# Performance work log

Hardware: AMD Instinct MI355X
Metric: run time of the kernel (lower is better)

Reference implementation:

```python
import jax, jax.numpy as jnp
import numpy as np

SCALE_BASE = 512.0
GAMMA = 0.96875

def xpos(x, downscale=False):
    # x: (B, L, d). XPOS = rotary embedding with exponential position-dependent scale.
    B, L, d = x.shape
    half = d // 2
    scale_vec = (jnp.arange(0, d, 2, dtype=jnp.float32) + 0.4 * d) / (1.4 * d)  # (half,)
    pos = jnp.arange(L, dtype=jnp.float32)
    scale = scale_vec[None, :] ** (pos[:, None] / SCALE_BASE)  # (L, half)
    if downscale:
        scale = 1.0 / scale
    inv_freq = 1.0 / (10000.0 ** (jnp.arange(half, dtype=jnp.float32) / half))
    sinusoid = pos[:, None] * inv_freq[None, :]  # (L, half)
    sin_s = jnp.repeat(jnp.sin(sinusoid) * scale, 2, axis=-1)  # duplicate_interleave -> (L, d)
    cos_s = jnp.repeat(jnp.cos(sinusoid) * scale, 2, axis=-1)
    x1, x2 = x[..., ::2], x[..., 1::2]
    rot = jnp.stack((-x2, x1), axis=-1).reshape(x.shape)  # rotate_every_two
    return x * cos_s + rot * sin_s

def decay_mask(L, gamma):
    n = jnp.arange(L)[:, None]
    m = jnp.arange(L)[None, :]
    diff = n - m
    expo = jnp.where(diff >= 0, diff, 0).astype(jnp.float32)
    return jnp.where(diff >= 0, gamma ** expo, 0.0)  # (L, L) causal decay

def setup_inputs() -> dict:
    key = jax.random.key(0)
    kx, kq, kk, kv = jax.random.split(key, 4)
    B, L, H = 4, 2048, 1024
    hs = 1024  # head_size == v_dim
    X = jax.random.normal(kx, (B, L, H), dtype=jnp.float32)
    W_Q = jax.random.normal(kq, (H, hs), dtype=jnp.float32) / H
    W_K = jax.random.normal(kk, (H, hs), dtype=jnp.float32) / H
    W_V = jax.random.normal(kv, (H, hs), dtype=jnp.float32) / H
    return {"X": X, "W_Q": W_Q, "W_K": W_K, "W_V": W_V}

def reference(X, W_Q, W_K, W_V):
    L = X.shape[1]
    Q = xpos(X @ W_Q)
    K = xpos(X @ W_K, downscale=True)
    V = X @ W_V
    D = decay_mask(L, GAMMA)
    ret = jnp.einsum('bnd,bmd->bnm', Q, K) * D[None]  # (B, L, L)
    return ret @ V
```

## Files before the change

### kernel.cpp

```cpp
#include <hip/hip_runtime.h>
#include <cmath>

typedef __attribute__((ext_vector_type(8))) short short8;
typedef __attribute__((ext_vector_type(4))) short short4v;
typedef __attribute__((ext_vector_type(4))) float float4v;
typedef unsigned short ushort_t;

#define LSEQ   2048
#define DMODEL 1024
#define BM 128
#define BN 128
#define BK 64
#define TPAD 136

#define L2GAMMA (-0.045803595f)
#define L2E4_512 (0.0259525632f)

__device__ __forceinline__ ushort_t f2b(float x) {
    union { float f; unsigned u; } v; v.f = x;
    unsigned r = v.u + 0x7fffu + ((v.u >> 16) & 1u);
    return (ushort_t)(r >> 16);
}

#define GLOAD_LDS16(gptr, lptr)                                                     \
    __builtin_amdgcn_global_load_lds(                                               \
        (const __attribute__((address_space(1))) unsigned int*)(gptr),              \
        (__attribute__((address_space(3))) unsigned int*)(lptr), 16, 0, 0)

#define MFMA16 __builtin_amdgcn_mfma_f32_16x16x32_bf16

__device__ __forceinline__ void gemm16_core(
    const ushort_t* __restrict__ Ag, int lda, int aRow0,
    const ushort_t* __restrict__ Bg, int ldb, int bRow0,
    int kDepth, ushort_t* As, ushort_t* Bs, float4v acc[4][4])
{
    const int tid  = threadIdx.x;
    const int wave = tid >> 6, lane = tid & 63;
    const int wm = wave >> 1, wn = wave & 1;
    const int l15 = lane & 15, l4g = lane >> 4, l7 = lane & 7;
    const int srow = lane >> 3;
    const int scol = ((lane & 7) ^ srow) * 8;

    const ushort_t* ap[4];
    const ushort_t* bp[4];
    #pragma unroll
    for (int L = 0; L < 4; ++L) {
        int r = (wave * 4 + L) * 8 + srow;
        ap[L] = Ag + (size_t)(aRow0 + r) * lda + scol;
        bp[L] = Bg + (size_t)(bRow0 + r) * ldb + scol;
    }
    const int ldst = srow * BK + (lane & 7) * 8;

    int aBase[2], bBase[2];
    #pragma unroll
    for (int h = 0; h < 2; ++h) {
        const int ch = ((h * 4 + l4g) ^ l7) * 8;
        aBase[h] = (wm * 64 + l15) * BK + ch;
        bBase[h] = (wn * 64 + l15) * BK + ch;
    }

    const int nt = kDepth / BK;
    #pragma unroll
    for (int L = 0; L < 4; ++L) {
        GLOAD_LDS16(ap[L], As + (wave * 4 + L) * (8 * BK) + ldst);
        GLOAD_LDS16(bp[L], Bs + (wave * 4 + L) * (8 * BK) + ldst);
        ap[L] += BK; bp[L] += BK;
    }

    for (int j = 0; j < nt; ++j) {
        const int cur = (j & 1) * (BM * BK);
        const int nxt = ((j + 1) & 1) * (BM * BK);
        if (j + 1 < nt) {
            #pragma unroll
            for (int L = 0; L < 4; ++L) {
                GLOAD_LDS16(ap[L], As + nxt + (wave * 4 + L) * (8 * BK) + ldst);
                GLOAD_LDS16(bp[L], Bs + nxt + (wave * 4 + L) * (8 * BK) + ldst);
                ap[L] += BK; bp[L] += BK;
            }
            asm volatile("s_waitcnt vmcnt(8)" ::: "memory");
        } else {
            asm volatile("s_waitcnt vmcnt(0)" ::: "memory");
        }
        __builtin_amdgcn_s_barrier();
        asm volatile("" ::: "memory");

        #pragma unroll
        for (int h = 0; h < 2; ++h) {
            short8 a[4], b[4];
            #pragma unroll
            for (int f = 0; f < 4; ++f) {
                a[f] = *(const short8*)(As + cur + aBase[h] + f * (16 * BK));
                b[f] = *(const short8*)(Bs + cur + bBase[h] + f * (16 * BK));
            }
            #pragma unroll
            for (int fr = 0; fr < 4; ++fr)
                #pragma unroll
                for (int fc = 0; fc < 4; ++fc)
                    acc[fr][fc] = MFMA16(a[fr], b[fc], acc[fr][fc], 0, 0, 0);
        }
        asm volatile("" ::: "memory");
        __builtin_amdgcn_s_barrier();
    }
}

__global__ __launch_bounds__(256) void prep_kernel(
    float2* __restrict__ T,
    const float* __restrict__ Wq, const float* __restrict__ Wk,
    const float* __restrict__ Wv, ushort_t* __restrict__ Wt,
    const float4* __restrict__ X, short4v* __restrict__ Xb, int n4)
{
    __shared__ float t[32][33];
    const int bid = blockIdx.x;
    if (bid < 8192) {
        int idx = bid * 256 + threadIdx.x;
        int l = idx & 2047;
        int p = (idx >> 11) & 511;
        int mode = idx >> 20;
        float sv = (2.0f * (float)p + 409.6f) * (1.0f / 1433.6f);
        float coeff = log2f(sv) * (1.0f / 512.0f) + L2GAMMA;
        float invf = exp2f(-(float)p * L2E4_512);
        float lf = (float)l;
        float s, c;
        sincosf(lf * invf, &s, &c);
        float g = exp2f((mode == 0 ? lf : -lf) * coeff);
        T[idx] = make_float2(c * g, s * g);
    } else if (bid < 11264) {
        const int wb = bid - 8192;
        const int bz = wb >> 10;
        const int rem = wb & 1023;
        const int by = rem >> 5, bx = rem & 31;
        const float* W = bz == 0 ? Wq : bz == 1 ? Wk : Wv;
        ushort_t* O = Wt + (size_t)bz * (DMODEL * DMODEL);
        const int x = threadIdx.x & 31, y = (threadIdx.x >> 5) * 4;
        const int k0 = by * 32, n0 = bx * 32;
        #pragma unroll
        for (int j = 0; j < 4; ++j)
            t[y + j][x] = W[(size_t)(k0 + y + j) * DMODEL + n0 + x];
        __syncthreads();
        #pragma unroll
        for (int j = 0; j < 4; ++j)
            O[(size_t)(n0 + y + j) * DMODEL + k0 + x] = f2b(t[x][y + j]);
    } else {
        int i = (bid - 11264) * 256 + threadIdx.x;
        if (i < n4) {
            float4 v = X[i];
            short4v o;
            o.x = (short)f2b(v.x); o.y = (short)f2b(v.y);
            o.z = (short)f2b(v.z); o.w = (short)f2b(v.w);
            Xb[i] = o;
        }
    }
}

__global__ __launch_bounds__(256) void qkv16_kernel(
    const ushort_t* __restrict__ Xb, const ushort_t* __restrict__ Wt,
    const float2* __restrict__ Tab,
    ushort_t* __restrict__ Q, ushort_t* __restrict__ Ko, ushort_t* __restrict__ Vt)
{
    __shared__ ushort_t smem[32768];
    ushort_t* As = smem;
    ushort_t* Bs = smem + 16384;

    const int nwg = gridDim.x;
    const int orig = blockIdx.x;
    const int lin = (orig & 7) * (nwg >> 3) + (orig >> 3);
    const int inner = lin & 63;
    const int sup = lin >> 6;
    const int c = (sup % 3) * 8 + (inner & 7);
    const int r = (sup / 3) * 8 + (inner >> 3);
    const int mode = c >> 3;
    const int c0 = (c & 7) * BN;
    const int row0 = r * BM;

    const int tid = threadIdx.x;
    const int wave = tid >> 6, lane = tid & 63;
    const int wm = wave >> 1, wn = wave & 1;
    const int l15 = lane & 15, l4g = lane >> 4, l7 = lane & 7;

    const int srow = lane >> 3;
    const int scol = ((lane & 7) ^ srow) * 8;
    const char* gA = (const char*)Xb;
    const char* gB = (const char*)(Wt + (size_t)mode * (DMODEL * DMODEL));
    unsigned aoff[4], boff[4];
    #pragma unroll
    for (int L = 0; L < 4; ++L) {
        const int rr = (wave * 4 + L) * 8 + srow;
        aoff[L] = (unsigned)(((row0 + rr) * DMODEL + scol) * 2);
        boff[L] = (unsigned)(((c0 + rr) * DMODEL + scol) * 2);
    }
    const int ldst = srow * BK + (lane & 7) * 8;

    int aBase[2], bBase[2];
    #pragma unroll
    for (int h = 0; h < 2; ++h) {
        const int ch = ((h * 4 + l4g) ^ l7) * 8;
        aBase[h] = (wm * 64 + l15) * BK + ch;
        bBase[h] = (wn * 64 + l15) * BK + ch;
    }

    float4v acc[4][4] = {};

    #pragma unroll
    for (int L = 0; L < 4; ++L) {
        GLOAD_LDS16(gA + aoff[L], As + (wave * 4 + L) * (8 * BK) + ldst);
        GLOAD_LDS16(gB + boff[L], Bs + (wave * 4 + L) * (8 * BK) + ldst);
        aoff[L] += 2 * BK; boff[L] += 2 * BK;
    }

    #pragma unroll 2
    for (int k = 0; k < 16; ++k) {
        const int cur = (k & 1) * (BM * BK);
        const int nxt = ((k + 1) & 1) * (BM * BK);
        if (k < 15) {
            #pragma unroll
            for (int L = 0; L < 4; ++L) {
                GLOAD_LDS16(gA + aoff[L], As + nxt + (wave * 4 + L) * (8 * BK) + ldst);
                GLOAD_LDS16(gB + boff[L], Bs + nxt + (wave * 4 + L) * (8 * BK) + ldst);
                aoff[L] += 2 * BK; boff[L] += 2 * BK;
            }
            asm volatile("s_waitcnt vmcnt(8)" ::: "memory");
        } else {
            asm volatile("s_waitcnt vmcnt(0)" ::: "memory");
        }
        __builtin_amdgcn_s_barrier();
        asm volatile("" ::: "memory");

        #pragma unroll
        for (int h = 0; h < 2; ++h) {
            short8 a[4], b[4];
            #pragma unroll
            for (int f = 0; f < 4; ++f) {
                a[f] = *(const short8*)(As + cur + aBase[h] + f * (16 * BK));
                b[f] = *(const short8*)(Bs + cur + bBase[h] + f * (16 * BK));
            }
            #pragma unroll
            for (int fr = 0; fr < 4; ++fr)
                #pragma unroll
                for (int fc = 0; fc < 4; ++fc)
                    acc[fr][fc] = MFMA16(a[fr], b[fc], acc[fr][fc], 0, 0, 0);
        }
        asm volatile("" ::: "memory");
        __builtin_amdgcn_s_barrier();
    }

    const int rB = row0 + wm * 64 + l4g * 4;
    const int cB = c0 + wn * 64 + l15;

    if (mode < 2) {
        ushort_t* O = (mode == 0) ? Q : Ko;
        const float2* Tm = Tab + (size_t)mode * (512 * 2048);
        #pragma unroll
        for (int fc = 0; fc < 4; ++fc) {
            const int col = cB + fc * 16;
            const float2* tp = Tm + ((size_t)(col >> 1) << 11);
            #pragma unroll
            for (int fr = 0; fr < 4; ++fr) {
                const int row = rB + fr * 16;
                const int l0 = row & 2047;
                float4 t01 = *(const float4*)(tp + l0);
                float4 t23 = *(const float4*)(tp + l0 + 2);
                float cs[8] = {t01.x, t01.y, t01.z, t01.w,
                               t23.x, t23.y, t23.z, t23.w};
                #pragma unroll
                for (int q = 0; q < 4; ++q) {
                    float v  = acc[fc][0][0];
                    v = acc[fr][fc][q];
                    float pv = __shfl_xor(v, 1);
                    float cc = cs[2 * q], ss = cs[2 * q + 1];
                    float res = (lane & 1) ? fmaf(v, cc, pv * ss)
                                           : fmaf(v, cc, -pv * ss);
                    O[(size_t)(row + q) * DMODEL + col] = f2b(res);
                }
            }
        }
    } else {
        __syncthreads();
        #pragma unroll
        for (int fc = 0; fc < 4; ++fc)
            #pragma unroll
            for (int fr = 0; fr < 4; ++fr) {
                short4v pk;
                pk.x = (short)f2b(acc[fr][fc][0]);
                pk.y = (short)f2b(acc[fr][fc][1]);
                pk.z = (short)f2b(acc[fr][fc][2]);
                pk.w = (short)f2b(acc[fr][fc][3]);
                *(short4v*)(smem + (wn * 64 + fc * 16 + l15) * TPAD
                                 + wm * 64 + fr * 16 + l4g * 4) = pk;
            }
        __syncthreads();
        const int t = threadIdx.x;
        const int colV = c0 + (t >> 1);
        const int lhalf = (t & 1) * 64;
        const int b = row0 >> 11, lpos0 = (row0 & 2047) + lhalf;
        #pragma unroll
        for (int i = 0; i < 8; ++i) {
            short8 vv = *(const short8*)(smem + (t >> 1) * TPAD + lhalf + i * 8);
            *(short8*)(Vt + (size_t)b * (LSEQ * DMODEL)
                          + (size_t)colV * LSEQ + lpos0 + i * 8) = vv;
        }
    }
}

__global__ __launch_bounds__(256) void score_kernel(
    const ushort_t* __restrict__ Q, const ushort_t* __restrict__ Kc,
    ushort_t* __restrict__ S)
{
    const int t = blockIdx.x, z = blockIdx.z;
    int bi, bj;
    if (t < 3) { bi = (t > 0); bj = t - (t > 0); }
    else { int u = t - 3; bi = 2 + u / 3; bj = bi - 2 + u % 3; }

    __shared__ ushort_t As[2 * BM * BK], Bs[2 * BN * BK];
    float4v acc[4][4] = {};
    const size_t zoff = (size_t)z * (LSEQ * DMODEL);
    gemm16_core(Q + zoff, DMODEL, bi * BM, Kc + zoff, DMODEL, bj * BN,
                DMODEL, As, Bs, acc);

    const int wave = threadIdx.x >> 6, lane = threadIdx.x & 63;
    const int wm = wave >> 1, wn = wave & 1;
    const int l15 = lane & 15, l4g = lane >> 4;
    const int nB = bi * BM + wm * 64 + l4g * 4;
    const int mB = bj * BN + wn * 64 + l15;
    ushort_t* Sz = S + (size_t)z * LSEQ * LSEQ;
    #pragma unroll
    for (int fr = 0; fr < 4; ++fr)
        #pragma unroll
        for (int fc = 0; fc < 4; ++fc) {
            const int m = mB + fc * 16;
            #pragma unroll
            for (int q = 0; q < 4; ++q) {
                const int n = nB + fr * 16 + q;
                Sz[(size_t)n * LSEQ + m] =
                    (m <= n) ? f2b(acc[fr][fc][q]) : (ushort_t)0;
            }
        }
}

__global__ __launch_bounds__(256) void av_kernel(
    const ushort_t* __restrict__ S, const ushort_t* __restrict__ Vt,
    float* __restrict__ Out)
{
    const int bx = blockIdx.x, bi = blockIdx.y, z = blockIdx.z;
    const int kLo = (bi >= 2) ? (bi - 2) * BM : 0;
    const int kW  = (bi + 1) * BM - kLo;
    __shared__ ushort_t As[2 * BM * BK], Bs[2 * BN * BK];
    float4v acc[4][4] = {};
    gemm16_core(S + (size_t)z * LSEQ * LSEQ + kLo, LSEQ, bi * BM,
                Vt + (size_t)z * (LSEQ * DMODEL) + kLo, LSEQ, bx * BN,
                kW, As, Bs, acc);

    const int wave = threadIdx.x >> 6, lane = threadIdx.x & 63;
    const int wm = wave >> 1, wn = wave & 1;
    const int l15 = lane & 15, l4g = lane >> 4;
    const int rB = bi * BM + wm * 64 + l4g * 4;
    const int cB = bx * BN + wn * 64 + l15;
    float* Oz = Out + (size_t)z * (LSEQ * DMODEL);
    #pragma unroll
    for (int fr = 0; fr < 4; ++fr)
        #pragma unroll
        for (int fc = 0; fc < 4; ++fc)
            #pragma unroll
            for (int q = 0; q < 4; ++q)
                Oz[(size_t)(rB + fr * 16 + q) * DMODEL + cB + fc * 16] =
                    acc[fr][fc][q];
}

extern "C" void kernel_launch(void* const* d_in, const int* in_sizes, int n_in,
                              void* d_out, int out_size, void* d_ws, size_t ws_size,
                              hipStream_t stream)
{
    const float* X  = (const float*)d_in[0];
    const float* Wq = (const float*)d_in[1];
    const float* Wk = (const float*)d_in[2];
    const float* Wv = (const float*)d_in[3];
    float* out = (float*)d_out;

    const size_t LH  = (size_t)LSEQ * DMODEL;
    const size_t WSZ = (size_t)DMODEL * DMODEL;
    const size_t SSZ = (size_t)LSEQ * LSEQ;
    const size_t TABN = (size_t)2 * 512 * 2048;

    size_t need4 = TABN * 8 + 2 * (3 * WSZ + 4 * (4 * LH + SSZ));
    const int bs = (ws_size >= need4) ? 4 : 1;

    float2* Tab = (float2*)d_ws;
    ushort_t* ws16 = (ushort_t*)(Tab + TABN);
    ushort_t* Wt = ws16;
    ushort_t* Xb = Wt + 3 * WSZ;
    ushort_t* Q  = Xb + (size_t)bs * LH;
    ushort_t* Kb = Q  + (size_t)bs * LH;
    ushort_t* Vt = Kb + (size_t)bs * LH;
    ushort_t* S  = Vt + (size_t)bs * LH;

    if (bs == 4) {
        prep_kernel<<<dim3(19456), 256, 0, stream>>>(
            Tab, Wq, Wk, Wv, Wt, (const float4*)X, (short4v*)Xb,
            (int)(4 * LH / 4));
        qkv16_kernel<<<dim3(24 * 4 * 16), 256, 0, stream>>>(
            Xb, Wt, Tab, Q, Kb, Vt);
        score_kernel<<<dim3(45, 1, 4), 256, 0, stream>>>(Q, Kb, S);
        av_kernel<<<dim3(8, 16, 4), 256, 0, stream>>>(S, Vt, out);
    } else {
        prep_kernel<<<dim3(11264), 256, 0, stream>>>(
            Tab, Wq, Wk, Wv, Wt, (const float4*)X, (short4v*)Xb, 0);
        for (int p = 0; p < 4; ++p) {
            const float* Xp = X + (size_t)p * LH;
            prep_kernel<<<dim3(2048), 256, 0, stream>>>(
                Tab, Wq, Wk, Wv, Wt,
                (const float4*)Xp, (short4v*)Xb, (int)(LH / 4));
            qkv16_kernel<<<dim3(24 * 16), 256, 0, stream>>>(
                Xb, Wt, Tab, Q, Kb, Vt);
            score_kernel<<<dim3(45, 1, 1), 256, 0, stream>>>(Q, Kb, S);
            av_kernel<<<dim3(8, 16, 1), 256, 0, stream>>>(S, Vt,
                out + (size_t)p * LH);
        }
    }
}
```

Baseline: 196.5 us.

## Split score tiles into 64-row blocks and stage AV output through LDS

```diff
diff --git a/kernel.cpp b/kernel.cpp
--- a/kernel.cpp
+++ b/kernel.cpp
@@ -263,8 +263,7 @@
                                t23.x, t23.y, t23.z, t23.w};
                 #pragma unroll
                 for (int q = 0; q < 4; ++q) {
-                    float v  = acc[fc][0][0];
-                    v = acc[fr][fc][q];
+                    float v  = acc[fr][fc][q];
                     float pv = __shfl_xor(v, 1);
                     float cc = cs[2 * q], ss = cs[2 * q + 1];
                     float res = (lane & 1) ? fmaf(v, cc, pv * ss)
@@ -306,24 +305,96 @@
     ushort_t* __restrict__ S)
 {
     const int t = blockIdx.x, z = blockIdx.z;
-    int bi, bj;
-    if (t < 3) { bi = (t > 0); bj = t - (t > 0); }
-    else { int u = t - 3; bi = 2 + u / 3; bj = bi - 2 + u % 3; }
-
-    __shared__ ushort_t As[2 * BM * BK], Bs[2 * BN * BK];
-    float4v acc[4][4] = {};
-    const size_t zoff = (size_t)z * (LSEQ * DMODEL);
-    gemm16_core(Q + zoff, DMODEL, bi * BM, Kc + zoff, DMODEL, bj * BN,
-                DMODEL, As, Bs, acc);
-
-    const int wave = threadIdx.x >> 6, lane = threadIdx.x & 63;
+    int ri, tj;
+    if (t < 2)      { ri = t; tj = 2; }
+    else if (t < 6) { int u = t - 2; ri = 2 + (u >> 1); tj = 1 + (u & 1); }
+    else            { int u = t - 6; ri = 4 + u / 3; tj = u % 3; }
+    const int n0 = ri * 64;
+    const int m0 = ((ri >> 1) - 2 + tj) * 128;
+
+    __shared__ ushort_t As[2 * 64 * BK];
+    __shared__ ushort_t Bs[2 * 128 * BK];
+
+    const int tid = threadIdx.x;
+    const int wave = tid >> 6, lane = tid & 63;
     const int wm = wave >> 1, wn = wave & 1;
-    const int l15 = lane & 15, l4g = lane >> 4;
-    const int nB = bi * BM + wm * 64 + l4g * 4;
-    const int mB = bj * BN + wn * 64 + l15;
+    const int l15 = lane & 15, l4g = lane >> 4, l7 = lane & 7;
+
+    const char* gA = (const char*)(Q + (size_t)z * ((size_t)LSEQ * DMODEL));
+    const char* gB = (const char*)(Kc + (size_t)z * ((size_t)LSEQ * DMODEL));
+    unsigned ao[2], bo[4];
+    int lA[2], lB[4];
+    #pragma unroll
+    for (int L = 0; L < 2; ++L) {
+        const int cc = tid + L * 256;
+        const int row = cc >> 3;
+        const int scol = ((cc & 7) ^ (row & 7)) * 8;
+        ao[L] = (unsigned)(((n0 + row) * DMODEL + scol) * 2);
+        lA[L] = cc * 8;
+    }
+    #pragma unroll
+    for (int L = 0; L < 4; ++L) {
+        const int cc = tid + L * 256;
+        const int row = cc >> 3;
+        const int scol = ((cc & 7) ^ (row & 7)) * 8;
+        bo[L] = (unsigned)(((m0 + row) * DMODEL + scol) * 2);
+        lB[L] = cc * 8;
+    }
+
+    int aBase[2], bBase[2];
+    #pragma unroll
+    for (int h = 0; h < 2; ++h) {
+        const int ch = ((h * 4 + l4g) ^ l7) * 8;
+        aBase[h] = (wm * 32 + l15) * BK + ch;
+        bBase[h] = (wn * 64 + l15) * BK + ch;
+    }
+
+    float4v acc[2][4] = {};
+
+    #pragma unroll
+    for (int L = 0; L < 2; ++L) { GLOAD_LDS16(gA + ao[L], As + lA[L]); ao[L] += 2 * BK; }
+    #pragma unroll
+    for (int L = 0; L < 4; ++L) { GLOAD_LDS16(gB + bo[L], Bs + lB[L]); bo[L] += 2 * BK; }
+
+    for (int j = 0; j < 16; ++j) {
+        const int curA = (j & 1) * (64 * BK),  curB = (j & 1) * (128 * BK);
+        const int nxtA = ((j + 1) & 1) * (64 * BK), nxtB = ((j + 1) & 1) * (128 * BK);
+        if (j < 15) {
+            #pragma unroll
+            for (int L = 0; L < 2; ++L) { GLOAD_LDS16(gA + ao[L], As + nxtA + lA[L]); ao[L] += 2 * BK; }
+            #pragma unroll
+            for (int L = 0; L < 4; ++L) { GLOAD_LDS16(gB + bo[L], Bs + nxtB + lB[L]); bo[L] += 2 * BK; }
+            asm volatile("s_waitcnt vmcnt(6)" ::: "memory");
+        } else {
+            asm volatile("s_waitcnt vmcnt(0)" ::: "memory");
+        }
+        __builtin_amdgcn_s_barrier();
+        asm volatile("" ::: "memory");
+
+        #pragma unroll
+        for (int h = 0; h < 2; ++h) {
+            short8 a[2], b[4];
+            #pragma unroll
+            for (int f = 0; f < 2; ++f)
+                a[f] = *(const short8*)(As + curA + aBase[h] + f * (16 * BK));
+            #pragma unroll
+            for (int f = 0; f < 4; ++f)
+                b[f] = *(const short8*)(Bs + curB + bBase[h] + f * (16 * BK));
+            #pragma unroll
+            for (int fr = 0; fr < 2; ++fr)
+                #pragma unroll
+                for (int fc = 0; fc < 4; ++fc)
+                    acc[fr][fc] = MFMA16(a[fr], b[fc], acc[fr][fc], 0, 0, 0);
+        }
+        asm volatile("" ::: "memory");
+        __builtin_amdgcn_s_barrier();
+    }
+
+    const int nB = n0 + wm * 32 + l4g * 4;
+    const int mB = m0 + wn * 64 + l15;
     ushort_t* Sz = S + (size_t)z * LSEQ * LSEQ;
     #pragma unroll
-    for (int fr = 0; fr < 4; ++fr)
+    for (int fr = 0; fr < 2; ++fr)
         #pragma unroll
         for (int fc = 0; fc < 4; ++fc) {
             const int m = mB + fc * 16;
@@ -343,26 +414,44 @@
     const int bx = blockIdx.x, bi = blockIdx.y, z = blockIdx.z;
     const int kLo = (bi >= 2) ? (bi - 2) * BM : 0;
     const int kW  = (bi + 1) * BM - kLo;
-    __shared__ ushort_t As[2 * BM * BK], Bs[2 * BN * BK];
+    __shared__ ushort_t smem[4 * BM * BK];
+    ushort_t* As = smem;
+    ushort_t* Bs = smem + 2 * BM * BK;
     float4v acc[4][4] = {};
     gemm16_core(S + (size_t)z * LSEQ * LSEQ + kLo, LSEQ, bi * BM,
-                Vt + (size_t)z * (LSEQ * DMODEL) + kLo, LSEQ, bx * BN,
+                Vt + (size_t)z * ((size_t)LSEQ * DMODEL) + kLo, LSEQ, bx * BN,
                 kW, As, Bs, acc);
 
-    const int wave = threadIdx.x >> 6, lane = threadIdx.x & 63;
+    const int tid = threadIdx.x;
+    const int wave = tid >> 6, lane = tid & 63;
     const int wm = wave >> 1, wn = wave & 1;
     const int l15 = lane & 15, l4g = lane >> 4;
-    const int rB = bi * BM + wm * 64 + l4g * 4;
-    const int cB = bx * BN + wn * 64 + l15;
-    float* Oz = Out + (size_t)z * (LSEQ * DMODEL);
+
+    float* T = (float*)smem;
     #pragma unroll
     for (int fr = 0; fr < 4; ++fr)
         #pragma unroll
-        for (int fc = 0; fc < 4; ++fc)
-            #pragma unroll
-            for (int q = 0; q < 4; ++q)
-                Oz[(size_t)(rB + fr * 16 + q) * DMODEL + cB + fc * 16] =
-                    acc[fr][fc][q];
+        for (int fc = 0; fc < 4; ++fc) {
+            const int lc = wn * 64 + fc * 16 + l15;
+            #pragma unroll
+            for (int q = 0; q < 4; ++q) {
+                const int lr = wm * 64 + fr * 16 + l4g * 4 + q;
+                const int sw = ((lr >> 2) & 15) << 2;
+                T[lr * 128 + (lc ^ sw)] = acc[fr][fc][q];
+            }
+        }
+    __syncthreads();
+
+    const int r = tid >> 1, chalf = (tid & 1) * 64;
+    const int sw = ((r >> 2) & 15) << 2;
+    float* Oz = Out + (size_t)z * ((size_t)LSEQ * DMODEL)
+              + (size_t)(bi * BM + r) * DMODEL + bx * BN + chalf;
+    #pragma unroll
+    for (int i = 0; i < 16; ++i) {
+        const int cc = chalf + i * 4;
+        float4 v = *(const float4*)&T[r * 128 + (cc ^ sw)];
+        *(float4*)&Oz[i * 4] = v;
+    }
 }
 
 extern "C" void kernel_launch(void* const* d_in, const int* in_sizes, int n_in,
@@ -398,7 +487,7 @@
             (int)(4 * LH / 4));
         qkv16_kernel<<<dim3(24 * 4 * 16), 256, 0, stream>>>(
             Xb, Wt, Tab, Q, Kb, Vt);
-        score_kernel<<<dim3(45, 1, 4), 256, 0, stream>>>(Q, Kb, S);
+        score_kernel<<<dim3(90, 1, 4), 256, 0, stream>>>(Q, Kb, S);
         av_kernel<<<dim3(8, 16, 4), 256, 0, stream>>>(S, Vt, out);
     } else {
         prep_kernel<<<dim3(11264), 256, 0, stream>>>(
@@ -410,7 +499,7 @@
                 (const float4*)Xp, (short4v*)Xb, (int)(LH / 4));
             qkv16_kernel<<<dim3(24 * 16), 256, 0, stream>>>(
                 Xb, Wt, Tab, Q, Kb, Vt);
-            score_kernel<<<dim3(45, 1, 1), 256, 0, stream>>>(Q, Kb, S);
+            score_kernel<<<dim3(90, 1, 1), 256, 0, stream>>>(Q, Kb, S);
             av_kernel<<<dim3(8, 16, 1), 256, 0, stream>>>(S, Vt,
                 out + (size_t)p * LH);
         }
```

Result: no change. 199.0 us (+1.2%).

## Add 256x256-tile QKV projection kernel with hand-scheduled LDS pipeline

Applied to the files above, without the earlier changes.

```diff
diff --git a/kernel.cpp b/kernel.cpp
--- a/kernel.cpp
+++ b/kernel.cpp
@@ -4,6 +4,7 @@
 typedef __attribute__((ext_vector_type(8))) short short8;
 typedef __attribute__((ext_vector_type(4))) short short4v;
 typedef __attribute__((ext_vector_type(4))) float float4v;
+typedef __attribute__((ext_vector_type(4))) int int4v;
 typedef unsigned short ushort_t;
 
 #define LSEQ   2048
@@ -28,6 +29,13 @@
         (__attribute__((address_space(3))) unsigned int*)(lptr), 16, 0, 0)
 
 #define MFMA16 __builtin_amdgcn_mfma_f32_16x16x32_bf16
+
+__device__ __forceinline__ short8 as8(int4v v) {
+    return __builtin_bit_cast(short8, v);
+}
+
+#define DSRN(dst, areg, imm) \
+    asm volatile("ds_read_b128 %0, %1 offset:%c2" : "=v"(dst) : "v"(areg), "n"(imm))
 
 __device__ __forceinline__ void gemm16_core(
     const ushort_t* __restrict__ Ag, int lda, int aRow0,
@@ -263,8 +271,7 @@
                                t23.x, t23.y, t23.z, t23.w};
                 #pragma unroll
                 for (int q = 0; q < 4; ++q) {
-                    float v  = acc[fc][0][0];
-                    v = acc[fr][fc][q];
+                    float v  = acc[fr][fc][q];
                     float pv = __shfl_xor(v, 1);
                     float cc = cs[2 * q], ss = cs[2 * q + 1];
                     float res = (lane & 1) ? fmaf(v, cc, pv * ss)
@@ -299,6 +306,203 @@
                           + (size_t)colV * LSEQ + lpos0 + i * 8) = vv;
         }
     }
+}
+
+__global__ __launch_bounds__(512) void qkv256_kernel(
+    const ushort_t* __restrict__ Xb, const ushort_t* __restrict__ Wt,
+    const float2* __restrict__ Tab,
+    ushort_t* __restrict__ Q, ushort_t* __restrict__ Ko, ushort_t* __restrict__ Vt)
+{
+    extern __shared__ ushort_t smem[];
+    const int tid  = threadIdx.x;
+    const int wave = tid >> 6, lane = tid & 63;
+    const int wm = wave >> 2, wn = wave & 3;
+    const int l15 = lane & 15, l4g = lane >> 4, l7 = lane & 7;
+
+    const int nwg = gridDim.x;
+    const int orig = blockIdx.x;
+    const int wg = (orig & 7) * (nwg >> 3) + (orig >> 3);
+    const int sup = wg >> 4, inner = wg & 15;
+    const int ct = (sup % 3) * 4 + (inner & 3);
+    const int rt = (sup / 3) * 4 + (inner >> 2);
+    const int mode = ct >> 2;
+    const int row0 = rt << 8;
+    const int c0m  = (ct & 3) << 8;
+
+    const char* gA = (const char*)Xb;
+    const char* gB = (const char*)(Wt + (size_t)mode * (DMODEL * DMODEL));
+
+    const int t8 = tid >> 3;
+    const int sw16 = ((tid & 7) ^ (t8 & 7)) << 4;
+    const unsigned oA = (unsigned)((row0 + t8) * 2048) + sw16;
+    const unsigned oB = (unsigned)((c0m + t8) * 2048) + sw16;
+    char* ldsT = (char*)smem + tid * 16;
+
+#define STG_A(d, h, kbyte) do {                                                  \
+    GLOAD_LDS16(gA + oA + (h) * 262144u + (kbyte),                               \
+                ldsT + (d) * 32768 + (h) * 16384);                               \
+    GLOAD_LDS16(gA + oA + (h) * 262144u + 131072u + (kbyte),                     \
+                ldsT + (d) * 32768 + (h) * 16384 + 8192);                        \
+} while (0)
+#define STG_B(d, h, kbyte) do {                                                  \
+    GLOAD_LDS16(gB + oB + (h) * 262144u + (kbyte),                               \
+                ldsT + 65536 + (d) * 32768 + (h) * 16384);                       \
+    GLOAD_LDS16(gB + oB + (h) * 262144u + 131072u + (kbyte),                     \
+                ldsT + 65536 + (d) * 32768 + (h) * 16384 + 8192);                \
+} while (0)
+
+    int vaA[2], vaB[2];
+    #pragma unroll
+    for (int kh = 0; kh < 2; ++kh) {
+        const int swz = (((kh * 4 + l4g) ^ l7) << 4);
+        vaA[kh] = wm * 16384 + l15 * 128 + swz;
+        vaB[kh] = 65536 + (wn >> 1) * 16384 + ((wn & 1) * 64 + l15) * 128 + swz;
+    }
+
+    float4v acc[8][4] = {};
+    int4v af[4][2];
+    int4v bf[4][2];
+
+#define RD_AQ(D, Qm) do {                                                        \
+    DSRN(af[0][0], vaA[0], (D) + (Qm) * 8192 + 0);                               \
+    DSRN(af[0][1], vaA[1], (D) + (Qm) * 8192 + 0);                               \
+    DSRN(af[1][0], vaA[0], (D) + (Qm) * 8192 + 2048);                            \
+    DSRN(af[1][1], vaA[1], (D) + (Qm) * 8192 + 2048);                            \
+    DSRN(af[2][0], vaA[0], (D) + (Qm) * 8192 + 4096);                            \
+    DSRN(af[2][1], vaA[1], (D) + (Qm) * 8192 + 4096);                            \
+    DSRN(af[3][0], vaA[0], (D) + (Qm) * 8192 + 6144);                            \
+    DSRN(af[3][1], vaA[1], (D) + (Qm) * 8192 + 6144);                            \
+} while (0)
+#define RD_BP(D, Pn) do {                                                        \
+    DSRN(bf[(Pn)*2+0][0], vaB[0], (D) + ((Pn)*2+0) * 2048);                      \
+    DSRN(bf[(Pn)*2+0][1], vaB[1], (D) + ((Pn)*2+0) * 2048);                      \
+    DSRN(bf[(Pn)*2+1][0], vaB[0], (D) + ((Pn)*2+1) * 2048);                      \
+    DSRN(bf[(Pn)*2+1][1], vaB[1], (D) + ((Pn)*2+1) * 2048);                      \
+} while (0)
+#define LGKM0 do { asm volatile("s_waitcnt lgkmcnt(0)" ::: "memory");            \
+                   __builtin_amdgcn_sched_barrier(0); } while (0)
+#define MM_Q(Qm, Pn) do {                                                        \
+    __builtin_amdgcn_s_setprio(1);                                               \
+    _Pragma("unroll")                                                            \
+    for (int fr = 0; fr < 4; ++fr)                                               \
+        _Pragma("unroll")                                                        \
+        for (int fc = 0; fc < 2; ++fc)                                           \
+            _Pragma("unroll")                                                    \
+            for (int kh = 0; kh < 2; ++kh)                                       \
+                acc[(Qm)*4+fr][(Pn)*2+fc] =                                      \
+                    MFMA16(as8(af[fr][kh]), as8(bf[(Pn)*2+fc][kh]),              \
+                           acc[(Qm)*4+fr][(Pn)*2+fc], 0, 0, 0);                  \
+    __builtin_amdgcn_s_setprio(0);                                               \
+} while (0)
+#define BAR __builtin_amdgcn_s_barrier()
+
+    STG_B(0, 0, 0);   STG_B(0, 1, 0);
+    STG_A(0, 0, 0);   STG_A(0, 1, 0);
+    STG_B(1, 0, 128); STG_B(1, 1, 128);
+
+    unsigned kb = 256;
+    for (int j = 0; j < 8; ++j) {
+        STG_A(1, 0, kb - 128);
+        asm volatile("s_waitcnt vmcnt(6)" ::: "memory");
+        BAR;
+        RD_AQ(0, 0); RD_BP(0, 0);
+        LGKM0; MM_Q(0, 0); BAR;
+        RD_BP(0, 1);
+        STG_A(1, 1, kb - 128);
+        BAR; LGKM0; MM_Q(0, 1); BAR;
+        RD_AQ(0, 1);
+        STG_B(0, 0, kb);
+        BAR; LGKM0; MM_Q(1, 0); BAR;
+        STG_B(0, 1, kb);
+        BAR; MM_Q(1, 1); BAR;
+        STG_A(0, 0, kb);
+        asm volatile("s_waitcnt vmcnt(6)" ::: "memory");
+        BAR;
+        RD_AQ(32768, 0); RD_BP(32768, 0);
+        LGKM0; MM_Q(0, 0); BAR;
+        RD_BP(32768, 1);
+        STG_A(0, 1, kb);
+        BAR; LGKM0; MM_Q(0, 1); BAR;
+        RD_AQ(32768, 1);
+        STG_B(1, 0, kb + 128);
+        BAR; LGKM0; MM_Q(1, 0); BAR;
+        STG_B(1, 1, kb + 128);
+        BAR; MM_Q(1, 1); BAR;
+
+        kb += 256;
+    }
+    asm volatile("s_waitcnt vmcnt(0)" ::: "memory");
+    BAR;
+
+    const int rB = row0 + wm * 128 + l4g * 4;
+    const int cB = c0m + wn * 64 + l15;
+
+    if (mode < 2) {
+        ushort_t* O = (mode == 0) ? Q : Ko;
+        const float2* Tm = Tab + (size_t)mode * (512 * 2048);
+        #pragma unroll
+        for (int fc = 0; fc < 4; ++fc) {
+            const int col = cB + fc * 16;
+            const float2* tp = Tm + ((size_t)(col >> 1) << 11);
+            #pragma unroll
+            for (int fr = 0; fr < 8; ++fr) {
+                const int row = rB + fr * 16;
+                const int l0 = row & 2047;
+                float4 t01 = *(const float4*)(tp + l0);
+                float4 t23 = *(const float4*)(tp + l0 + 2);
+                float cs[8] = {t01.x, t01.y, t01.z, t01.w,
+                               t23.x, t23.y, t23.z, t23.w};
+                #pragma unroll
+                for (int q = 0; q < 4; ++q) {
+                    float v  = acc[fr][fc][q];
+                    float pv = __shfl_xor(v, 1);
+                    float cc = cs[2 * q], ss = cs[2 * q + 1];
+                    float res = (lane & 1) ? fmaf(v, cc, pv * ss)
+                                           : fmaf(v, cc, -pv * ss);
+                    O[(size_t)(row + q) * DMODEL + col] = f2b(res);
+                }
+            }
+        }
+    } else {
+        const int bidx = row0 >> 11, lpos0 = row0 & 2047;
+        #pragma unroll
+        for (int ph = 0; ph < 2; ++ph) {
+            if ((wn >> 1) == ph) {
+                const int colL = (wn & 1) * 64 + l15;
+                const int rowL = wm * 128 + l4g * 4;
+                #pragma unroll
+                for (int fc = 0; fc < 4; ++fc)
+                    #pragma unroll
+                    for (int fr = 0; fr < 8; ++fr) {
+                        short4v pk;
+                        pk.x = (short)f2b(acc[fr][fc][0]);
+                        pk.y = (short)f2b(acc[fr][fc][1]);
+                        pk.z = (short)f2b(acc[fr][fc][2]);
+                        pk.w = (short)f2b(acc[fr][fc][3]);
+                        *(short4v*)(smem + (size_t)(colL + fc * 16) * 264
+                                         + rowL + fr * 16) = pk;
+                    }
+            }
+            __syncthreads();
+            const int tc = tid >> 2, qtr = tid & 3;
+            const int colV = c0m + ph * 128 + tc;
+            #pragma unroll
+            for (int i = 0; i < 8; ++i) {
+                short8 vv = *(const short8*)(smem + (size_t)tc * 264
+                                                  + qtr * 64 + i * 8);
+                *(short8*)(Vt + (size_t)bidx * (LSEQ * DMODEL)
+                              + (size_t)colV * LSEQ + lpos0 + qtr * 64 + i * 8) = vv;
+            }
+            __syncthreads();
+        }
+    }
+#undef STG_A
+#undef STG_B
+#undef RD_AQ
+#undef RD_BP
+#undef LGKM0
+#undef MM_Q
+#undef BAR
 }
 
 __global__ __launch_bounds__(256) void score_kernel(
@@ -346,7 +550,7 @@
     __shared__ ushort_t As[2 * BM * BK], Bs[2 * BN * BK];
     float4v acc[4][4] = {};
     gemm16_core(S + (size_t)z * LSEQ * LSEQ + kLo, LSEQ, bi * BM,
-                Vt + (size_t)z * (LSEQ * DMODEL) + kLo, LSEQ, bx * BN,
+                Vt + (size_t)z * ((size_t)LSEQ * DMODEL) + kLo, LSEQ, bx * BN,
                 kW, As, Bs, acc);
 
     const int wave = threadIdx.x >> 6, lane = threadIdx.x & 63;
@@ -354,7 +558,7 @@
     const int l15 = lane & 15, l4g = lane >> 4;
     const int rB = bi * BM + wm * 64 + l4g * 4;
     const int cB = bx * BN + wn * 64 + l15;
-    float* Oz = Out + (size_t)z * (LSEQ * DMODEL);
+    float* Oz = Out + (size_t)z * ((size_t)LSEQ * DMODEL);
     #pragma unroll
     for (int fr = 0; fr < 4; ++fr)
         #pragma unroll
@@ -392,12 +596,24 @@
     ushort_t* Vt = Kb + (size_t)bs * LH;
     ushort_t* S  = Vt + (size_t)bs * LH;
 
+    static int qkv256_ok = -1;
+    if (qkv256_ok < 0) {
+        hipError_t e = hipFuncSetAttribute(
+            reinterpret_cast<const void*>(qkv256_kernel),
+            hipFuncAttributeMaxDynamicSharedMemorySize, 131072);
+        qkv256_ok = (e == hipSuccess) ? 1 : 0;
+    }
+
     if (bs == 4) {
         prep_kernel<<<dim3(19456), 256, 0, stream>>>(
             Tab, Wq, Wk, Wv, Wt, (const float4*)X, (short4v*)Xb,
             (int)(4 * LH / 4));
-        qkv16_kernel<<<dim3(24 * 4 * 16), 256, 0, stream>>>(
-            Xb, Wt, Tab, Q, Kb, Vt);
+        if (qkv256_ok)
+            qkv256_kernel<<<dim3(384), 512, 131072, stream>>>(
+                Xb, Wt, Tab, Q, Kb, Vt);
+        else
+            qkv16_kernel<<<dim3(24 * 4 * 16), 256, 0, stream>>>(
+                Xb, Wt, Tab, Q, Kb, Vt);
         score_kernel<<<dim3(45, 1, 4), 256, 0, stream>>>(Q, Kb, S);
         av_kernel<<<dim3(8, 16, 4), 256, 0, stream>>>(S, Vt, out);
     } else {
@@ -408,8 +624,12 @@
             prep_kernel<<<dim3(2048), 256, 0, stream>>>(
                 Tab, Wq, Wk, Wv, Wt,
                 (const float4*)Xp, (short4v*)Xb, (int)(LH / 4));
-            qkv16_kernel<<<dim3(24 * 16), 256, 0, stream>>>(
-                Xb, Wt, Tab, Q, Kb, Vt);
+            if (qkv256_ok)
+                qkv256_kernel<<<dim3(96), 512, 131072, stream>>>(
+                    Xb, Wt, Tab, Q, Kb, Vt);
+            else
+                qkv16_kernel<<<dim3(24 * 16), 256, 0, stream>>>(
+                    Xb, Wt, Tab, Q, Kb, Vt);
             score_kernel<<<dim3(45, 1, 1), 256, 0, stream>>>(Q, Kb, S);
             av_kernel<<<dim3(8, 16, 1), 256, 0, stream>>>(S, Vt,
                 out + (size_t)p * LH);
```

After: 213.8 us. 1.09x slower.
